# Kernel tuning notes

Hardware: AMD Instinct MI355X
Metric: run time of the kernel (lower is better)

Reference implementation:

```python
import jax, jax.numpy as jnp
import numpy as np
from jax import lax

DN = ('NCHW', 'OIHW', 'NCHW')


def conv3x3(x, w, b):
    return lax.conv_general_dilated(x, w, (1, 1), 'SAME', dimension_numbers=DN) + b[None, :, None, None]


def conv1x1(x, w, b):
    # w: [O, I] -> pointwise conv
    return jnp.einsum('oi,bihw->bohw', w, x) + b[None, :, None, None]


def sft(x0, x1, sc0w, sc0b, sc1w, sc1b, sh0w, sh0b, sh1w, sh1b):
    scale = conv1x1(jax.nn.leaky_relu(conv1x1(x1, sc0w, sc0b), 0.1), sc1w, sc1b)
    shift = conv1x1(jax.nn.leaky_relu(conv1x1(x1, sh0w, sh0b), 0.1), sh1w, sh1b)
    return x0 * (scale + 1.0) + shift


def deform_conv(x, offset, w, b):
    # torchvision DeformConv2d, 3x3, stride 1, pad 1, dilation 1, no mask.
    B, C, H, W = x.shape
    O = w.shape[0]
    K = 9
    off = offset.reshape(B, K, 2, H, W)  # (dy, dx) per kernel tap
    ki = jnp.arange(3, dtype=x.dtype) - 1.0
    ky = jnp.repeat(ki, 3)  # [9]
    kx = jnp.tile(ki, 3)
    hh = jnp.arange(H, dtype=x.dtype)
    ww = jnp.arange(W, dtype=x.dtype)
    py = off[:, :, 0] + hh[None, None, :, None] + ky[None, :, None, None]  # [B,K,H,W]
    px = off[:, :, 1] + ww[None, None, None, :] + kx[None, :, None, None]
    y0f = jnp.floor(py)
    x0f = jnp.floor(px)
    wy = (py - y0f)[:, None]  # [B,1,K,H,W]
    wx = (px - x0f)[:, None]
    y0 = y0f.astype(jnp.int32)
    x0i = x0f.astype(jnp.int32)
    x_flat = x.reshape(B, C, H * W)

    def gather(iy, ix):
        valid = (iy >= 0) & (iy < H) & (ix >= 0) & (ix < W)
        idx = (jnp.clip(iy, 0, H - 1) * W + jnp.clip(ix, 0, W - 1)).reshape(B, K * H * W)
        vals = jax.vmap(lambda xf, ii: xf[:, ii])(x_flat, idx)  # [B,C,K*H*W]
        return vals.reshape(B, C, K, H, W) * valid[:, None].astype(x.dtype)

    v00 = gather(y0, x0i)
    v01 = gather(y0, x0i + 1)
    v10 = gather(y0 + 1, x0i)
    v11 = gather(y0 + 1, x0i + 1)
    samp = (v00 * (1 - wy) * (1 - wx) + v01 * (1 - wy) * wx
            + v10 * wy * (1 - wx) + v11 * wy * wx)  # [B,C,K,H,W]
    return jnp.einsum('bckhw,ock->bohw', samp, w.reshape(O, C, K)) + b[None, :, None, None]


def setup_inputs() -> dict:
    key = jax.random.key(0)
    ks = jax.random.split(key, 32)
    B, C0, C1, H, W = 4, 128, 32, 96, 96
    f32 = jnp.float32
    d = {
        'x0': jax.random.normal(ks[0], (B, C0, H, W), f32),
        'x1': jax.random.normal(ks[1], (B, C1, H, W), f32),
        'w_off': jax.random.normal(ks[2], (18, C0, 3, 3), f32) * 0.02,
        'b_off': jnp.zeros((18,), f32),
        's1_sc0_w': jax.random.normal(ks[3], (C0, C1), f32) * 0.05,
        's1_sc0_b': jnp.zeros((C0,), f32),
        's1_sc1_w': jax.random.normal(ks[4], (C0, C0), f32) * 0.05,
        's1_sc1_b': jnp.zeros((C0,), f32),
        's1_sh0_w': jax.random.normal(ks[5], (C0, C1), f32) * 0.05,
        's1_sh0_b': jnp.zeros((C0,), f32),
        's1_sh1_w': jax.random.normal(ks[6], (C0, C0), f32) * 0.05,
        's1_sh1_b': jnp.zeros((C0,), f32),
        'w_d1': jax.random.normal(ks[7], (C0, C0, 3, 3), f32) * 0.03,
        'b_d1': jnp.zeros((C0,), f32),
        's2_sc0_w': jax.random.normal(ks[8], (C0, C1), f32) * 0.05,
        's2_sc0_b': jnp.zeros((C0,), f32),
        's2_sc1_w': jax.random.normal(ks[9], (C0, C0), f32) * 0.05,
        's2_sc1_b': jnp.zeros((C0,), f32),
        's2_sh0_w': jax.random.normal(ks[10], (C0, C1), f32) * 0.05,
        's2_sh0_b': jnp.zeros((C0,), f32),
        's2_sh1_w': jax.random.normal(ks[11], (C0, C0), f32) * 0.05,
        's2_sh1_b': jnp.zeros((C0,), f32),
        'w_d2': jax.random.normal(ks[12], (C0, C0, 3, 3), f32) * 0.03,
        'b_d2': jnp.zeros((C0,), f32),
    }
    return d


def reference(x0, x1, w_off, b_off,
              s1_sc0_w, s1_sc0_b, s1_sc1_w, s1_sc1_b,
              s1_sh0_w, s1_sh0_b, s1_sh1_w, s1_sh1_b,
              w_d1, b_d1,
              s2_sc0_w, s2_sc0_b, s2_sc1_w, s2_sc1_b,
              s2_sh0_w, s2_sh0_b, s2_sh1_w, s2_sh1_b,
              w_d2, b_d2):
    off = conv3x3(x0, w_off, b_off)
    fea = sft(x0, x1, s1_sc0_w, s1_sc0_b, s1_sc1_w, s1_sc1_b,
              s1_sh0_w, s1_sh0_b, s1_sh1_w, s1_sh1_b)
    fea = jax.nn.relu(deform_conv(fea, off, w_d1, b_d1))
    fea = sft(fea, x1, s2_sc0_w, s2_sc0_b, s2_sc1_w, s2_sc1_b,
              s2_sh0_w, s2_sh0_b, s2_sh1_w, s2_sh1_b)
    fea = deform_conv(fea, off, w_d2, b_d2)
    return x0 + fea
```

## Files before the change

kernel.cpp:

```cpp
#include <hip/hip_runtime.h>

typedef unsigned short u16;
typedef unsigned int   u32;
typedef __attribute__((ext_vector_type(8))) _Float16 f16x8;
typedef __attribute__((ext_vector_type(2))) float f32x2;
typedef __attribute__((ext_vector_type(4))) float f32x4;
typedef __attribute__((ext_vector_type(4))) unsigned int u32x4;

constexpr int B_  = 4;
constexpr int C0  = 128;
constexpr int C1  = 32;
constexpr int H_  = 96;
constexpr int W_  = 96;
constexpr int HW  = H_ * W_;
constexpr int PT  = 64;
constexpr int TPB = HW / PT;
constexpr int NTILE = B_ * TPB;

__device__ inline u16 f2h(float f) {
    _Float16 h = (_Float16)f;
    return __builtin_bit_cast(u16, h);
}

__global__ __launch_bounds__(256) void k_prep(
    const float* __restrict__ w_off,
    const float* __restrict__ wd1,  const float* __restrict__ wd2,
    const float* __restrict__ s1c0, const float* __restrict__ s1h0,
    const float* __restrict__ s2c0, const float* __restrict__ s2h0,
    const float* __restrict__ s1c1, const float* __restrict__ s1h1,
    const float* __restrict__ s2c1, const float* __restrict__ s2h1,
    float* __restrict__ wofft, u16* __restrict__ wdhi, u16* __restrict__ wdlo,
    u16* __restrict__ w0h,     u16* __restrict__ w1h)
{
    int t = blockIdx.x * 256 + threadIdx.x;
    if (t < C0 * 18 * 9) {
        int c = t / 162, r = t % 162, o = r / 9, tap = r % 9;
        wofft[t] = w_off[(o * C0 + c) * 9 + tap];
    }
    if (t < 2 * 9 * C0 * C0) {
        int d = t / (9 * C0 * C0), r = t % (9 * C0 * C0);
        int k = r / (C0 * C0), r2 = r % (C0 * C0), o = r2 / C0, c = r2 % C0;
        const float* wsrc = d ? wd2 : wd1;
        float wv = wsrc[(o * C0 + c) * 9 + k];
        _Float16 hi = (_Float16)wv;
        float rr = wv - (float)hi;
        wdhi[t] = __builtin_bit_cast(u16, hi);
        wdlo[t] = f2h(rr);
    }
    if (t < 4 * C0 * C1) {
        int m = t / (C0 * C1), i = t % (C0 * C1);
        const float* s = (m == 0) ? s1c0 : (m == 1) ? s1h0 : (m == 2) ? s2c0 : s2h0;
        w0h[t] = f2h(s[i]);
    }
    if (t < 4 * C0 * C0) {
        int m = t / (C0 * C0), i = t % (C0 * C0);
        const float* s = (m == 0) ? s1c1 : (m == 1) ? s1h1 : (m == 2) ? s2c1 : s2h1;
        w1h[t] = f2h(s[i]);
    }
}

__global__ __launch_bounds__(256) void k_conv_off(
    const float* __restrict__ x0, const float* __restrict__ wofft,
    const float* __restrict__ boff, float* __restrict__ off)
{
    int bx = blockIdx.x;
    int b  = bx / TPB;
    int p0 = (bx % TPB) * PT;
    int tid = threadIdx.x;
    int p   = tid & 63;
    int cq  = __builtin_amdgcn_readfirstlane(tid >> 6);
    int pos = p0 + p;
    int h = pos / W_, w = pos % W_;

    float acc[18];
#pragma unroll
    for (int o = 0; o < 18; ++o) acc[o] = 0.f;

    for (int cc = 0; cc < 32; ++cc) {
        int c = cq * 32 + cc;
        const float* xb = x0 + ((size_t)(b * C0 + c)) * HW;
        float v[9];
#pragma unroll
        for (int t = 0; t < 9; ++t) {
            int dy = t / 3 - 1, dx = t % 3 - 1;
            int hy = h + dy, wx = w + dx;
            bool ok = (hy >= 0) & (hy < H_) & (wx >= 0) & (wx < W_);
            v[t] = ok ? xb[hy * W_ + wx] : 0.f;
        }
        const float* wr = wofft + c * 162;
#pragma unroll
        for (int o = 0; o < 18; ++o)
#pragma unroll
            for (int t = 0; t < 9; ++t)
                acc[o] = fmaf(wr[o * 9 + t], v[t], acc[o]);
    }

    __shared__ float red[4][18][PT];
#pragma unroll
    for (int o = 0; o < 18; ++o) red[cq][o][p] = acc[o];
    __syncthreads();
    for (int idx = tid; idx < 18 * PT; idx += 256) {
        int o = idx / PT, pp = idx % PT;
        float s = red[0][o][pp] + red[1][o][pp] + red[2][o][pp] + red[3][o][pp]
                + boff[o];
        off[((size_t)(b * 18 + o)) * HW + p0 + pp] = s;
    }
}

template <int XSRC>
__global__ __launch_bounds__(512) void k_sft_mma(
    const float* __restrict__ xf,
    const float* __restrict__ xT,
    const float* __restrict__ x1,
    const u16* __restrict__ w0s, const u16* __restrict__ w0h,
    const u16* __restrict__ w1s, const u16* __restrict__ w1h,
    const float* __restrict__ b0s, const float* __restrict__ b0h,
    const float* __restrict__ b1s, const float* __restrict__ b1h,
    float* __restrict__ outT)
{
    __shared__ __align__(16) u16   x1t[64 * 32];
    __shared__ __align__(16) u16   hidt[2][64 * 128];
    __shared__ __align__(16) float outt[64 * 128];

    int bx = blockIdx.x, b = bx / TPB, p0 = (bx % TPB) * PT;
    int tid = threadIdx.x, l = tid & 63;
    int w = __builtin_amdgcn_readfirstlane(tid >> 6);
    f32x4 zz = {0.f, 0.f, 0.f, 0.f};

    for (int i = tid; i < C1 * PT; i += 512) {
        int ch = i >> 6, pos = i & 63;
        float v = x1[((size_t)(b * C1 + ch)) * HW + p0 + pos];
        x1t[pos * 32 + (ch ^ ((pos & 3) << 3))] = f2h(v);
    }
    __syncthreads();

    {
        int mt = w & 3, br = w >> 2;
        int pos = mt * 16 + (l & 15);
        int koff = (l >> 4) * 8;
        f16x8 a = *(const f16x8*)&x1t[pos * 32 + (koff ^ ((pos & 3) << 3))];
        const u16* w0 = br ? w0h : w0s;
        const float* bb = br ? b0h : b0s;
        u16* hrow = hidt[br];
#pragma unroll
        for (int nt = 0; nt < 8; ++nt) {
            int n = nt * 16 + (l & 15);
            f16x8 bfr = *(const f16x8*)&w0[n * 32 + koff];
            f32x4 h = __builtin_amdgcn_mfma_f32_16x16x32_f16(a, bfr, zz, 0, 0, 0);
            float bv = bb[n];
#pragma unroll
            for (int r = 0; r < 4; ++r) {
                float hv = h[r] + bv;
                hv = hv > 0.f ? hv : 0.1f * hv;
                int prow = mt * 16 + (l >> 4) * 4 + r;
                hrow[prow * 128 + (n ^ ((prow & 7) << 3))] = f2h(hv);
            }
        }
    }
    __syncthreads();

    f32x4 accS[4], accH[4];
#pragma unroll
    for (int nt = 0; nt < 4; ++nt) { accS[nt] = zz; accH[nt] = zz; }
    int mt = w & 3, nh = w >> 2;
    int pos = mt * 16 + (l & 15);
#pragma unroll
    for (int ks = 0; ks < 4; ++ks) {
        int kb = ks * 32 + (l >> 4) * 8;
        f16x8 aS = *(const f16x8*)&hidt[0][pos * 128 + (kb ^ ((pos & 7) << 3))];
        f16x8 aH = *(const f16x8*)&hidt[1][pos * 128 + (kb ^ ((pos & 7) << 3))];
#pragma unroll
        for (int nt = 0; nt < 4; ++nt) {
            int n = nh * 64 + nt * 16 + (l & 15);
            f16x8 bS = *(const f16x8*)&w1s[n * 128 + kb];
            f16x8 bH = *(const f16x8*)&w1h[n * 128 + kb];
            accS[nt] = __builtin_amdgcn_mfma_f32_16x16x32_f16(aS, bS, accS[nt], 0, 0, 0);
            accH[nt] = __builtin_amdgcn_mfma_f32_16x16x32_f16(aH, bH, accH[nt], 0, 0, 0);
        }
    }

#pragma unroll
    for (int nt = 0; nt < 4; ++nt) {
        int n = nh * 64 + nt * 16 + (l & 15);
        float scb = b1s[n], shb = b1h[n];
        float xv[4];
        if (XSRC == 0) {
            const float* xp = xf + ((size_t)(b * C0 + n)) * HW + p0 + mt * 16 + (l >> 4) * 4;
            f32x4 x4 = *(const f32x4*)xp;
#pragma unroll
            for (int r = 0; r < 4; ++r) xv[r] = x4[r];
        } else {
#pragma unroll
            for (int r = 0; r < 4; ++r)
                xv[r] = xT[((size_t)(b * HW + p0 + mt * 16 + (l >> 4) * 4 + r)) * C0 + n];
        }
#pragma unroll
        for (int r = 0; r < 4; ++r) {
            float scale = accS[nt][r] + scb + 1.f;
            float shift = accH[nt][r] + shb;
            outt[(mt * 16 + (l >> 4) * 4 + r) * 128 + n] = xv[r] * scale + shift;
        }
    }
    __syncthreads();

    float* dst = outT + ((size_t)(b * HW + p0)) * C0;
    for (int i = tid; i < 2048; i += 512)
        *(f32x4*)&dst[i * 4] = *(const f32x4*)&outt[i * 4];
}

template <int MODE>
__global__ __launch_bounds__(512, 4) void k_deform4(
    const float* __restrict__ srcT,
    const float* __restrict__ off,
    const u16* __restrict__ whi,
    const u16* __restrict__ wlo,
    const float* __restrict__ bias,
    const float* __restrict__ x0,
    float* __restrict__ outF,
    float* __restrict__ outT)
{
    constexpr int S = 136;
    __shared__ __align__(16) u16   smem[4 * 64 * S];
    __shared__ __align__(16) u16   cidx[9 * 64 * 4];
    __shared__ __align__(16) float cwt[9 * 64 * 2];
    u16* a_hi = smem;
    u16* a_lo = smem + 64 * S;
    u16* b_hi = smem + 2 * 64 * S;
    u16* b_lo = smem + 3 * 64 * S;

    int bx = blockIdx.x;
    bx = (bx & 7) * (NTILE / 8) + (bx >> 3);
    int b = bx / TPB, p0 = (bx % TPB) * PT;
    int tid = threadIdx.x, l = tid & 63;
    int w = __builtin_amdgcn_readfirstlane(tid >> 6);
    f32x4 zz = {0.f, 0.f, 0.f, 0.f};

    for (int e = tid; e < 9 * 64; e += 512) {
        int k = e >> 6, pp = e & 63;
        int pos = p0 + pp, h = pos / W_, wc = pos % W_;
        float dy = off[((size_t)(b * 18 + 2 * k)) * HW + pos];
        float dx = off[((size_t)(b * 18 + 2 * k + 1)) * HW + pos];
        float py = dy + (float)(h + k / 3 - 1);
        float px = dx + (float)(wc + k % 3 - 1);
        float yf = floorf(py), xf = floorf(px);
        int y0 = (int)yf, x0i = (int)xf;
        cwt[e * 2]     = py - yf;
        cwt[e * 2 + 1] = px - xf;
        int iy0 = min(max(y0, 0), H_ - 1),     iy1 = min(max(y0 + 1, 0), H_ - 1);
        int ix0 = min(max(x0i, 0), W_ - 1),    ix1 = min(max(x0i + 1, 0), W_ - 1);
        bool vy0 = (y0 >= 0) & (y0 < H_),      vy1 = (y0 + 1 >= 0) & (y0 + 1 < H_);
        bool vx0 = (x0i >= 0) & (x0i < W_),    vx1 = (x0i + 1 >= 0) & (x0i + 1 < W_);
        cidx[e * 4 + 0] = (u16)(iy0 * W_ + ix0) | ((vy0 & vx0) ? 0x8000 : 0);
        cidx[e * 4 + 1] = (u16)(iy0 * W_ + ix1) | ((vy0 & vx1) ? 0x8000 : 0);
        cidx[e * 4 + 2] = (u16)(iy1 * W_ + ix0) | ((vy1 & vx0) ? 0x8000 : 0);
        cidx[e * 4 + 3] = (u16)(iy1 * W_ + ix1) | ((vy1 & vx1) ? 0x8000 : 0);
    }
    __syncthreads();

    f32x4 acc[2][2];
#pragma unroll
    for (int hf = 0; hf < 2; ++hf)
#pragma unroll
        for (int nt = 0; nt < 2; ++nt) acc[hf][nt] = zz;

    int mt = w & 3, ng = w >> 2;
    int pos_r = mt * 16 + (l & 15);
    int so = tid >> 3, sp = tid & 7;
    const float* base  = srcT + (size_t)b * HW * C0;
    const float* lbase = base + 2 * l;

    f32x2 gv[8][4];

#define ISSUE(KK)                                                             \
    {                                                                         \
        int ek = (KK) * 64 + w * 8;                                           \
        _Pragma("unroll")                                                     \
        for (int i = 0; i < 8; ++i) {                                         \
            int e = ek + i;                                                   \
            u32 c01 = *(const u32*)&cidx[e * 4];                              \
            u32 c23 = *(const u32*)&cidx[e * 4 + 2];                          \
            gv[i][0] = *(const f32x2*)(lbase + (size_t)(c01 & 0x3fffu) * C0); \
            gv[i][1] = *(const f32x2*)(lbase + (size_t)((c01 >> 16) & 0x3fffu) * C0); \
            gv[i][2] = *(const f32x2*)(lbase + (size_t)(c23 & 0x3fffu) * C0); \
            gv[i][3] = *(const f32x2*)(lbase + (size_t)((c23 >> 16) & 0x3fffu) * C0); \
        }                                                                     \
    }

#define COMMIT(KK)                                                            \
    {                                                                         \
        int ek = (KK) * 64 + w * 8;                                           \
        _Pragma("unroll")                                                     \
        for (int i = 0; i < 8; ++i) {                                         \
            int e = ek + i, pp = w * 8 + i;                                   \
            u32 c01 = *(const u32*)&cidx[e * 4];                              \
            u32 c23 = *(const u32*)&cidx[e * 4 + 2];                          \
            float wy = cwt[e * 2], wx = cwt[e * 2 + 1];                       \
            float aa  = wy * wx;                                              \
            float w11 = (c23 & 0x80000000u) ? aa : 0.f;                       \
            float w10 = (c23 & 0x8000u) ? (wy - aa) : 0.f;                    \
            float w01 = (c01 & 0x80000000u) ? (wx - aa) : 0.f;                \
            float w00 = (c01 & 0x8000u) ? (1.f - wy - wx + aa) : 0.f;         \
            float s0 = gv[i][0][0] * w00 + gv[i][1][0] * w01                  \
                     + gv[i][2][0] * w10 + gv[i][3][0] * w11;                 \
            float s1 = gv[i][0][1] * w00 + gv[i][1][1] * w01                  \
                     + gv[i][2][1] * w10 + gv[i][3][1] * w11;                 \
            _Float16 h0 = (_Float16)s0, h1 = (_Float16)s1;                    \
            float r0 = s0 - (float)h0, r1 = s1 - (float)h1;                   \
            u32 hv = (u32)__builtin_bit_cast(u16, h0)                         \
                   | ((u32)__builtin_bit_cast(u16, h1) << 16);                \
            u32 lv = (u32)f2h(r0) | ((u32)f2h(r1) << 16);                     \
            *(u32*)&a_hi[pp * S + 2 * l] = hv;                                \
            *(u32*)&a_lo[pp * S + 2 * l] = lv;                                \
        }                                                                     \
    }

#define STAGEB(KK, HF)                                                        \
    {                                                                         \
        int orow = (HF) * 64 + so;                                            \
        const u16* sh = whi + ((size_t)(KK) * C0 + orow) * C0 + sp * 16;      \
        const u16* sl = wlo + ((size_t)(KK) * C0 + orow) * C0 + sp * 16;      \
        _Pragma("unroll")                                                     \
        for (int j = 0; j < 2; ++j) {                                         \
            *(u32x4*)&b_hi[so * S + sp * 16 + j * 8] = *(const u32x4*)&sh[j * 8]; \
            *(u32x4*)&b_lo[so * S + sp * 16 + j * 8] = *(const u32x4*)&sl[j * 8]; \
        }                                                                     \
    }

#define MFMA_HALF(HF)                                                         \
    {                                                                         \
        _Pragma("unroll")                                                     \
        for (int ks = 0; ks < 4; ++ks) {                                      \
            int kb = ks * 32 + (l >> 4) * 8;                                  \
            int ai = pos_r * S + kb;                                          \
            f16x8 ah = *(const f16x8*)&a_hi[ai];                              \
            f16x8 al = *(const f16x8*)&a_lo[ai];                              \
            _Pragma("unroll")                                                 \
            for (int nt = 0; nt < 2; ++nt) {                                  \
                int orow = ng * 32 + nt * 16 + (l & 15);                      \
                int bi = orow * S + kb;                                       \
                f16x8 bh = *(const f16x8*)&b_hi[bi];                          \
                f16x8 bl = *(const f16x8*)&b_lo[bi];                          \
                acc[HF][nt] = __builtin_amdgcn_mfma_f32_16x16x32_f16(ah, bh, acc[HF][nt], 0, 0, 0); \
                acc[HF][nt] = __builtin_amdgcn_mfma_f32_16x16x32_f16(al, bh, acc[HF][nt], 0, 0, 0); \
                acc[HF][nt] = __builtin_amdgcn_mfma_f32_16x16x32_f16(ah, bl, acc[HF][nt], 0, 0, 0); \
            }                                                                 \
        }                                                                     \
    }

    ISSUE(0)
    for (int k = 0; k < 9; ++k) {
        COMMIT(k)
        STAGEB(k, 0)
        __syncthreads();
        if (k < 8) ISSUE(k + 1)
        MFMA_HALF(0)
        __syncthreads();
        STAGEB(k, 1)
        __syncthreads();
        MFMA_HALF(1)
        __syncthreads();
    }
#undef ISSUE
#undef COMMIT
#undef STAGEB
#undef MFMA_HALF

    if (MODE == 0) {
        float* otile = (float*)smem;
#pragma unroll
        for (int hf = 0; hf < 2; ++hf)
#pragma unroll
            for (int nt = 0; nt < 2; ++nt) {
                int o = hf * 64 + ng * 32 + nt * 16 + (l & 15);
                float bv = bias[o];
#pragma unroll
                for (int r = 0; r < 4; ++r) {
                    float v = acc[hf][nt][r] + bv;
                    v = v > 0.f ? v : 0.f;
                    otile[(mt * 16 + (l >> 4) * 4 + r) * 132 + o] = v;
                }
            }
        __syncthreads();
        float* dst = outT + ((size_t)(b * HW + p0)) * C0;
        for (int i = tid; i < 2048; i += 512) {
            int row = i >> 5, c = i & 31;
            *(f32x4*)&dst[row * 128 + c * 4] = *(const f32x4*)&otile[row * 132 + c * 4];
        }
    } else {
#pragma unroll
        for (int hf = 0; hf < 2; ++hf)
#pragma unroll
            for (int nt = 0; nt < 2; ++nt) {
                int o = hf * 64 + ng * 32 + nt * 16 + (l & 15);
                float bv = bias[o];
                size_t base_o = ((size_t)(b * C0 + o)) * HW + p0 + mt * 16 + (l >> 4) * 4;
                f32x4 x4 = *(const f32x4*)(x0 + base_o);
                f32x4 ov;
#pragma unroll
                for (int r = 0; r < 4; ++r) ov[r] = acc[hf][nt][r] + bv + x4[r];
                *(f32x4*)(outF + base_o) = ov;
            }
    }
}

constexpr size_t WB_OFF   = 0;
constexpr size_t WB_WOFFT = 2654208;
constexpr size_t WB_W0H   = 2737152;
constexpr size_t WB_W1H   = 2769920;
constexpr size_t WB_WDHI  = 2900992;
constexpr size_t WB_WDLO  = 4080640;
constexpr size_t WB_TA    = 5260288;
constexpr size_t WB_TB    = 24134656;

extern "C" void kernel_launch(void* const* d_in, const int* in_sizes, int n_in,
                              void* d_out, int out_size, void* d_ws, size_t ws_size,
                              hipStream_t stream)
{
    const float* x0      = (const float*)d_in[0];
    const float* x1      = (const float*)d_in[1];
    const float* w_off   = (const float*)d_in[2];
    const float* b_off   = (const float*)d_in[3];
    const float* s1_sc0w = (const float*)d_in[4];
    const float* s1_sc0b = (const float*)d_in[5];
    const float* s1_sc1w = (const float*)d_in[6];
    const float* s1_sc1b = (const float*)d_in[7];
    const float* s1_sh0w = (const float*)d_in[8];
    const float* s1_sh0b = (const float*)d_in[9];
    const float* s1_sh1w = (const float*)d_in[10];
    const float* s1_sh1b = (const float*)d_in[11];
    const float* w_d1    = (const float*)d_in[12];
    const float* b_d1    = (const float*)d_in[13];
    const float* s2_sc0w = (const float*)d_in[14];
    const float* s2_sc0b = (const float*)d_in[15];
    const float* s2_sc1w = (const float*)d_in[16];
    const float* s2_sc1b = (const float*)d_in[17];
    const float* s2_sh0w = (const float*)d_in[18];
    const float* s2_sh0b = (const float*)d_in[19];
    const float* s2_sh1w = (const float*)d_in[20];
    const float* s2_sh1b = (const float*)d_in[21];
    const float* w_d2    = (const float*)d_in[22];
    const float* b_d2    = (const float*)d_in[23];

    char* wsb = (char*)d_ws;
    float* off   = (float*)(wsb + WB_OFF);
    float* wofft = (float*)(wsb + WB_WOFFT);
    u16*   w0h   = (u16*)(wsb + WB_W0H);
    u16*   w1h   = (u16*)(wsb + WB_W1H);
    u16*   wdhi  = (u16*)(wsb + WB_WDHI);
    u16*   wdlo  = (u16*)(wsb + WB_WDLO);
    float* TA    = (float*)(wsb + WB_TA);
    float* TB    = (float*)(wsb + WB_TB);

    k_prep<<<1152, 256, 0, stream>>>(w_off, w_d1, w_d2,
                                     s1_sc0w, s1_sh0w, s2_sc0w, s2_sh0w,
                                     s1_sc1w, s1_sh1w, s2_sc1w, s2_sh1w,
                                     wofft, wdhi, wdlo, w0h, w1h);
    k_conv_off<<<NTILE, 256, 0, stream>>>(x0, wofft, b_off, off);
    k_sft_mma<0><<<NTILE, 512, 0, stream>>>(x0, nullptr, x1,
                                            w0h, w0h + 4096,
                                            w1h, w1h + 16384,
                                            s1_sc0b, s1_sh0b, s1_sc1b, s1_sh1b, TA);
    k_deform4<0><<<NTILE, 512, 0, stream>>>(TA, off, wdhi, wdlo, b_d1,
                                            nullptr, nullptr, TB);
    k_sft_mma<1><<<NTILE, 512, 0, stream>>>(nullptr, TB, x1,
                                            w0h + 8192, w0h + 12288,
                                            w1h + 32768, w1h + 49152,
                                            s2_sc0b, s2_sh0b, s2_sc1b, s2_sh1b, TA);
    k_deform4<1><<<NTILE, 512, 0, stream>>>(TA, off, wdhi + 9 * 16384, wdlo + 9 * 16384,
                                            b_d2, x0, (float*)d_out, nullptr);
}
```

Before: 373.3 us.

## Software-pipeline deform-conv gathers and weight loads across MFMA halves

Splits the per-tap bilinear gather into two half-batches held in separate register sets and prefetches the fp16 weight tiles into registers one stage ahead. The second half of the gather and the next weight half are issued before the MFMA phases, so global-memory latency overlaps with matrix work. Scheduling barriers keep the compiler from reordering the loads past the synchronisations. This cuts the peak gather register footprint from 8 taps to two sets of 4 but adds 16 registers for weights, which may affect occupancy under the 512x4 launch bound.

```diff
diff --git a/kernel.cpp b/kernel.cpp
--- a/kernel.cpp
+++ b/kernel.cpp
@@ -209,7 +209,7 @@
 }
 
 template <int MODE>
-__global__ __launch_bounds__(512, 4) void k_deform4(
+__global__ __launch_bounds__(512, 4) void k_deform5(
     const float* __restrict__ srcT,
     const float* __restrict__ off,
     const u16* __restrict__ whi,
@@ -269,29 +269,30 @@
     const float* base  = srcT + (size_t)b * HW * C0;
     const float* lbase = base + 2 * l;
 
-    f32x2 gv[8][4];
-
-#define ISSUE(KK)                                                             \
+    f32x2 gv1[4][4], gv2[4][4];
+    u32x4 rbh0, rbh1, rbl0, rbl1;
+
+#define ISSUE_A(DST, KK, IOFF)                                                \
     {                                                                         \
-        int ek = (KK) * 64 + w * 8;                                           \
+        int ek = (KK) * 64 + w * 8 + (IOFF);                                  \
         _Pragma("unroll")                                                     \
-        for (int i = 0; i < 8; ++i) {                                         \
+        for (int i = 0; i < 4; ++i) {                                         \
             int e = ek + i;                                                   \
             u32 c01 = *(const u32*)&cidx[e * 4];                              \
             u32 c23 = *(const u32*)&cidx[e * 4 + 2];                          \
-            gv[i][0] = *(const f32x2*)(lbase + (size_t)(c01 & 0x3fffu) * C0); \
-            gv[i][1] = *(const f32x2*)(lbase + (size_t)((c01 >> 16) & 0x3fffu) * C0); \
-            gv[i][2] = *(const f32x2*)(lbase + (size_t)(c23 & 0x3fffu) * C0); \
-            gv[i][3] = *(const f32x2*)(lbase + (size_t)((c23 >> 16) & 0x3fffu) * C0); \
+            DST[i][0] = *(const f32x2*)(lbase + (size_t)(c01 & 0x3fffu) * C0);\
+            DST[i][1] = *(const f32x2*)(lbase + (size_t)((c01 >> 16) & 0x3fffu) * C0); \
+            DST[i][2] = *(const f32x2*)(lbase + (size_t)(c23 & 0x3fffu) * C0);\
+            DST[i][3] = *(const f32x2*)(lbase + (size_t)((c23 >> 16) & 0x3fffu) * C0); \
         }                                                                     \
     }
 
-#define COMMIT(KK)                                                            \
+#define COMMIT_HALF(SRC, KK, IOFF)                                            \
     {                                                                         \
-        int ek = (KK) * 64 + w * 8;                                           \
+        int ek = (KK) * 64 + w * 8 + (IOFF);                                  \
         _Pragma("unroll")                                                     \
-        for (int i = 0; i < 8; ++i) {                                         \
-            int e = ek + i, pp = w * 8 + i;                                   \
+        for (int i = 0; i < 4; ++i) {                                         \
+            int e = ek + i, pp = w * 8 + (IOFF) + i;                          \
             u32 c01 = *(const u32*)&cidx[e * 4];                              \
             u32 c23 = *(const u32*)&cidx[e * 4 + 2];                          \
             float wy = cwt[e * 2], wx = cwt[e * 2 + 1];                       \
@@ -300,10 +301,10 @@
             float w10 = (c23 & 0x8000u) ? (wy - aa) : 0.f;                    \
             float w01 = (c01 & 0x80000000u) ? (wx - aa) : 0.f;                \
             float w00 = (c01 & 0x8000u) ? (1.f - wy - wx + aa) : 0.f;         \
-            float s0 = gv[i][0][0] * w00 + gv[i][1][0] * w01                  \
-                     + gv[i][2][0] * w10 + gv[i][3][0] * w11;                 \
-            float s1 = gv[i][0][1] * w00 + gv[i][1][1] * w01                  \
-                     + gv[i][2][1] * w10 + gv[i][3][1] * w11;                 \
+            float s0 = SRC[i][0][0] * w00 + SRC[i][1][0] * w01                \
+                     + SRC[i][2][0] * w10 + SRC[i][3][0] * w11;               \
+            float s1 = SRC[i][0][1] * w00 + SRC[i][1][1] * w01                \
+                     + SRC[i][2][1] * w10 + SRC[i][3][1] * w11;               \
             _Float16 h0 = (_Float16)s0, h1 = (_Float16)s1;                    \
             float r0 = s0 - (float)h0, r1 = s1 - (float)h1;                   \
             u32 hv = (u32)__builtin_bit_cast(u16, h0)                         \
@@ -314,16 +315,21 @@
         }                                                                     \
     }
 
-#define STAGEB(KK, HF)                                                        \
+#define ISSUE_B(KK, HF)                                                       \
     {                                                                         \
         int orow = (HF) * 64 + so;                                            \
         const u16* sh = whi + ((size_t)(KK) * C0 + orow) * C0 + sp * 16;      \
         const u16* sl = wlo + ((size_t)(KK) * C0 + orow) * C0 + sp * 16;      \
-        _Pragma("unroll")                                                     \
-        for (int j = 0; j < 2; ++j) {                                         \
-            *(u32x4*)&b_hi[so * S + sp * 16 + j * 8] = *(const u32x4*)&sh[j * 8]; \
-            *(u32x4*)&b_lo[so * S + sp * 16 + j * 8] = *(const u32x4*)&sl[j * 8]; \
-        }                                                                     \
+        rbh0 = *(const u32x4*)&sh[0];  rbh1 = *(const u32x4*)&sh[8];          \
+        rbl0 = *(const u32x4*)&sl[0];  rbl1 = *(const u32x4*)&sl[8];          \
+    }
+
+#define WRITE_B()                                                             \
+    {                                                                         \
+        *(u32x4*)&b_hi[so * S + sp * 16]     = rbh0;                          \
+        *(u32x4*)&b_hi[so * S + sp * 16 + 8] = rbh1;                          \
+        *(u32x4*)&b_lo[so * S + sp * 16]     = rbl0;                          \
+        *(u32x4*)&b_lo[so * S + sp * 16 + 8] = rbl1;                          \
     }
 
 #define MFMA_HALF(HF)                                                         \
@@ -347,22 +353,32 @@
         }                                                                     \
     }
 
-    ISSUE(0)
+    ISSUE_A(gv1, 0, 0)
+    ISSUE_A(gv2, 0, 4)
+    ISSUE_B(0, 0)
+
     for (int k = 0; k < 9; ++k) {
-        COMMIT(k)
-        STAGEB(k, 0)
+        COMMIT_HALF(gv1, k, 0)
+        COMMIT_HALF(gv2, k, 4)
+        WRITE_B()
+        ISSUE_B(k, 1)
+        if (k < 8) ISSUE_A(gv1, k + 1, 0)
+        __builtin_amdgcn_sched_barrier(0);
         __syncthreads();
-        if (k < 8) ISSUE(k + 1)
         MFMA_HALF(0)
         __syncthreads();
-        STAGEB(k, 1)
+        WRITE_B()
+        if (k < 8) { ISSUE_B(k + 1, 0) }
+        if (k < 8) { ISSUE_A(gv2, k + 1, 4) }
+        __builtin_amdgcn_sched_barrier(0);
         __syncthreads();
         MFMA_HALF(1)
         __syncthreads();
     }
-#undef ISSUE
-#undef COMMIT
-#undef STAGEB
+#undef ISSUE_A
+#undef COMMIT_HALF
+#undef ISSUE_B
+#undef WRITE_B
 #undef MFMA_HALF
 
     if (MODE == 0) {
@@ -460,12 +476,12 @@
                                             w0h, w0h + 4096,
                                             w1h, w1h + 16384,
                                             s1_sc0b, s1_sh0b, s1_sc1b, s1_sh1b, TA);
-    k_deform4<0><<<NTILE, 512, 0, stream>>>(TA, off, wdhi, wdlo, b_d1,
+    k_deform5<0><<<NTILE, 512, 0, stream>>>(TA, off, wdhi, wdlo, b_d1,
                                             nullptr, nullptr, TB);
     k_sft_mma<1><<<NTILE, 512, 0, stream>>>(nullptr, TB, x1,
                                             w0h + 8192, w0h + 12288,
                                             w1h + 32768, w1h + 49152,
                                             s2_sc0b, s2_sh0b, s2_sc1b, s2_sh1b, TA);
-    k_deform4<1><<<NTILE, 512, 0, stream>>>(TA, off, wdhi + 9 * 16384, wdlo + 9 * 16384,
+    k_deform5<1><<<NTILE, 512, 0, stream>>>(TA, off, wdhi + 9 * 16384, wdlo + 9 * 16384,
                                             b_d2, x0, (float*)d_out, nullptr);
 }
```

Measured after the change: 365.2 us. -2.2%, faster.

## Double-buffer deform conv tiles with register-staged weights and fewer barriers

Applied to the files above, without the earlier changes.

The deformable conv kernel now double-buffers the gathered A tile and stages the full 128-row weight slice in LDS once per tap. Weights and gathers for tap k+2 are prefetched into registers while MFMAs run on tap k, which cuts the per-tap barrier count from four to two, and MFMA sections are raised in priority with setprio. The warp layout changes to 2x4 with 32x32 output per warp, increasing A/B fragment reuse. The SFT kernel drops its LDS output staging in favour of direct strided global stores and gets a 6-waves occupancy hint. The risks are higher LDS and register use lowering occupancy, and uncoalesced stores in the SFT kernel.

```diff
diff --git a/kernel.cpp b/kernel.cpp
--- a/kernel.cpp
+++ b/kernel.cpp
@@ -108,7 +108,7 @@
 }
 
 template <int XSRC>
-__global__ __launch_bounds__(512) void k_sft_mma(
+__global__ __launch_bounds__(512, 6) void k_sft_mma(
     const float* __restrict__ xf,
     const float* __restrict__ xT,
     const float* __restrict__ x1,
@@ -118,9 +118,8 @@
     const float* __restrict__ b1s, const float* __restrict__ b1h,
     float* __restrict__ outT)
 {
-    __shared__ __align__(16) u16   x1t[64 * 32];
-    __shared__ __align__(16) u16   hidt[2][64 * 128];
-    __shared__ __align__(16) float outt[64 * 128];
+    __shared__ __align__(16) u16 x1t[64 * 32];
+    __shared__ __align__(16) u16 hidt[2][64 * 128];
 
     int bx = blockIdx.x, b = bx / TPB, p0 = (bx % TPB) * PT;
     int tid = threadIdx.x, l = tid & 63;
@@ -198,18 +197,14 @@
         for (int r = 0; r < 4; ++r) {
             float scale = accS[nt][r] + scb + 1.f;
             float shift = accH[nt][r] + shb;
-            outt[(mt * 16 + (l >> 4) * 4 + r) * 128 + n] = xv[r] * scale + shift;
-        }
-    }
-    __syncthreads();
-
-    float* dst = outT + ((size_t)(b * HW + p0)) * C0;
-    for (int i = tid; i < 2048; i += 512)
-        *(f32x4*)&dst[i * 4] = *(const f32x4*)&outt[i * 4];
+            outT[((size_t)(b * HW + p0 + mt * 16 + (l >> 4) * 4 + r)) * C0 + n]
+                = xv[r] * scale + shift;
+        }
+    }
 }
 
 template <int MODE>
-__global__ __launch_bounds__(512, 4) void k_deform4(
+__global__ __launch_bounds__(512) void k_deform9(
     const float* __restrict__ srcT,
     const float* __restrict__ off,
     const u16* __restrict__ whi,
@@ -220,13 +215,10 @@
     float* __restrict__ outT)
 {
     constexpr int S = 136;
-    __shared__ __align__(16) u16   smem[4 * 64 * S];
+    __shared__ __align__(16) u16   a_buf[2][2][64 * S];
+    __shared__ __align__(16) u16   b_buf[2][128 * S];
     __shared__ __align__(16) u16   cidx[9 * 64 * 4];
     __shared__ __align__(16) float cwt[9 * 64 * 2];
-    u16* a_hi = smem;
-    u16* a_lo = smem + 64 * S;
-    u16* b_hi = smem + 2 * 64 * S;
-    u16* b_lo = smem + 3 * 64 * S;
 
     int bx = blockIdx.x;
     bx = (bx & 7) * (NTILE / 8) + (bx >> 3);
@@ -259,19 +251,19 @@
 
     f32x4 acc[2][2];
 #pragma unroll
-    for (int hf = 0; hf < 2; ++hf)
-#pragma unroll
-        for (int nt = 0; nt < 2; ++nt) acc[hf][nt] = zz;
-
-    int mt = w & 3, ng = w >> 2;
-    int pos_r = mt * 16 + (l & 15);
-    int so = tid >> 3, sp = tid & 7;
-    const float* base  = srcT + (size_t)b * HW * C0;
-    const float* lbase = base + 2 * l;
+    for (int ms = 0; ms < 2; ++ms)
+#pragma unroll
+        for (int ns = 0; ns < 2; ++ns) acc[ms][ns] = zz;
+
+    int mh = w & 1, ng = w >> 1;
+    int kq = l >> 4;
+    const float* lbase = srcT + (size_t)b * HW * C0 + 2 * l;
+    int wrow = tid >> 2, wseg = tid & 3;
 
     f32x2 gv[8][4];
-
-#define ISSUE(KK)                                                             \
+    u32x4 wbh[4], wbl[4];
+
+#define ISSUE_G(KK)                                                           \
     {                                                                         \
         int ek = (KK) * 64 + w * 8;                                           \
         _Pragma("unroll")                                                     \
@@ -284,9 +276,22 @@
             gv[i][2] = *(const f32x2*)(lbase + (size_t)(c23 & 0x3fffu) * C0); \
             gv[i][3] = *(const f32x2*)(lbase + (size_t)((c23 >> 16) & 0x3fffu) * C0); \
         }                                                                     \
-    }
-
-#define COMMIT(KK)                                                            \
+        __builtin_amdgcn_sched_barrier(0);                                    \
+    }
+
+#define ISSUE_W(KK)                                                           \
+    {                                                                         \
+        const u16* sh = whi + (size_t)(KK) * 16384 + wrow * 128 + wseg * 32;  \
+        const u16* sl = wlo + (size_t)(KK) * 16384 + wrow * 128 + wseg * 32;  \
+        _Pragma("unroll")                                                     \
+        for (int j = 0; j < 4; ++j) {                                         \
+            wbh[j] = *(const u32x4*)&sh[j * 8];                               \
+            wbl[j] = *(const u32x4*)&sl[j * 8];                               \
+        }                                                                     \
+        __builtin_amdgcn_sched_barrier(0);                                    \
+    }
+
+#define COMMIT_A(KK, D)                                                       \
     {                                                                         \
         int ek = (KK) * 64 + w * 8;                                           \
         _Pragma("unroll")                                                     \
@@ -309,75 +314,96 @@
             u32 hv = (u32)__builtin_bit_cast(u16, h0)                         \
                    | ((u32)__builtin_bit_cast(u16, h1) << 16);                \
             u32 lv = (u32)f2h(r0) | ((u32)f2h(r1) << 16);                     \
-            *(u32*)&a_hi[pp * S + 2 * l] = hv;                                \
-            *(u32*)&a_lo[pp * S + 2 * l] = lv;                                \
+            *(u32*)&a_buf[D][0][pp * S + 2 * l] = hv;                         \
+            *(u32*)&a_buf[D][1][pp * S + 2 * l] = lv;                         \
         }                                                                     \
     }
 
-#define STAGEB(KK, HF)                                                        \
-    {                                                                         \
-        int orow = (HF) * 64 + so;                                            \
-        const u16* sh = whi + ((size_t)(KK) * C0 + orow) * C0 + sp * 16;      \
-        const u16* sl = wlo + ((size_t)(KK) * C0 + orow) * C0 + sp * 16;      \
-        _Pragma("unroll")                                                     \
-        for (int j = 0; j < 2; ++j) {                                         \
-            *(u32x4*)&b_hi[so * S + sp * 16 + j * 8] = *(const u32x4*)&sh[j * 8]; \
-            *(u32x4*)&b_lo[so * S + sp * 16 + j * 8] = *(const u32x4*)&sl[j * 8]; \
-        }                                                                     \
-    }
-
-#define MFMA_HALF(HF)                                                         \
+#define WRITE_B()                                                             \
     {                                                                         \
         _Pragma("unroll")                                                     \
-        for (int ks = 0; ks < 4; ++ks) {                                      \
-            int kb = ks * 32 + (l >> 4) * 8;                                  \
-            int ai = pos_r * S + kb;                                          \
-            f16x8 ah = *(const f16x8*)&a_hi[ai];                              \
-            f16x8 al = *(const f16x8*)&a_lo[ai];                              \
-            _Pragma("unroll")                                                 \
-            for (int nt = 0; nt < 2; ++nt) {                                  \
-                int orow = ng * 32 + nt * 16 + (l & 15);                      \
-                int bi = orow * S + kb;                                       \
-                f16x8 bh = *(const f16x8*)&b_hi[bi];                          \
-                f16x8 bl = *(const f16x8*)&b_lo[bi];                          \
-                acc[HF][nt] = __builtin_amdgcn_mfma_f32_16x16x32_f16(ah, bh, acc[HF][nt], 0, 0, 0); \
-                acc[HF][nt] = __builtin_amdgcn_mfma_f32_16x16x32_f16(al, bh, acc[HF][nt], 0, 0, 0); \
-                acc[HF][nt] = __builtin_amdgcn_mfma_f32_16x16x32_f16(ah, bl, acc[HF][nt], 0, 0, 0); \
-            }                                                                 \
+        for (int j = 0; j < 4; ++j) {                                         \
+            *(u32x4*)&b_buf[0][wrow * S + wseg * 32 + j * 8] = wbh[j];        \
+            *(u32x4*)&b_buf[1][wrow * S + wseg * 32 + j * 8] = wbl[j];        \
         }                                                                     \
     }
 
-    ISSUE(0)
+#define MFMA_KS(KS, D)                                                        \
+    {                                                                         \
+        int kb = (KS) * 32 + kq * 8;                                          \
+        f16x8 ah0 = *(const f16x8*)&a_buf[D][0][(mh * 32 + (l & 15)) * S + kb];      \
+        f16x8 al0 = *(const f16x8*)&a_buf[D][1][(mh * 32 + (l & 15)) * S + kb];      \
+        f16x8 ah1 = *(const f16x8*)&a_buf[D][0][(mh * 32 + 16 + (l & 15)) * S + kb]; \
+        f16x8 al1 = *(const f16x8*)&a_buf[D][1][(mh * 32 + 16 + (l & 15)) * S + kb]; \
+        f16x8 bh0 = *(const f16x8*)&b_buf[0][(ng * 32 + (l & 15)) * S + kb];         \
+        f16x8 bl0 = *(const f16x8*)&b_buf[1][(ng * 32 + (l & 15)) * S + kb];         \
+        f16x8 bh1 = *(const f16x8*)&b_buf[0][(ng * 32 + 16 + (l & 15)) * S + kb];    \
+        f16x8 bl1 = *(const f16x8*)&b_buf[1][(ng * 32 + 16 + (l & 15)) * S + kb];    \
+        acc[0][0] = __builtin_amdgcn_mfma_f32_16x16x32_f16(ah0, bh0, acc[0][0], 0, 0, 0); \
+        acc[0][1] = __builtin_amdgcn_mfma_f32_16x16x32_f16(ah0, bh1, acc[0][1], 0, 0, 0); \
+        acc[1][0] = __builtin_amdgcn_mfma_f32_16x16x32_f16(ah1, bh0, acc[1][0], 0, 0, 0); \
+        acc[1][1] = __builtin_amdgcn_mfma_f32_16x16x32_f16(ah1, bh1, acc[1][1], 0, 0, 0); \
+        acc[0][0] = __builtin_amdgcn_mfma_f32_16x16x32_f16(al0, bh0, acc[0][0], 0, 0, 0); \
+        acc[0][1] = __builtin_amdgcn_mfma_f32_16x16x32_f16(al0, bh1, acc[0][1], 0, 0, 0); \
+        acc[1][0] = __builtin_amdgcn_mfma_f32_16x16x32_f16(al1, bh0, acc[1][0], 0, 0, 0); \
+        acc[1][1] = __builtin_amdgcn_mfma_f32_16x16x32_f16(al1, bh1, acc[1][1], 0, 0, 0); \
+        acc[0][0] = __builtin_amdgcn_mfma_f32_16x16x32_f16(ah0, bl0, acc[0][0], 0, 0, 0); \
+        acc[0][1] = __builtin_amdgcn_mfma_f32_16x16x32_f16(ah0, bl1, acc[0][1], 0, 0, 0); \
+        acc[1][0] = __builtin_amdgcn_mfma_f32_16x16x32_f16(ah1, bl0, acc[1][0], 0, 0, 0); \
+        acc[1][1] = __builtin_amdgcn_mfma_f32_16x16x32_f16(ah1, bl1, acc[1][1], 0, 0, 0); \
+    }
+
+#define LGKM_BAR                                                              \
+    asm volatile("s_waitcnt lgkmcnt(0)" ::: "memory");                        \
+    __builtin_amdgcn_s_barrier();
+
+    ISSUE_G(0)
+    ISSUE_W(0)
+    COMMIT_A(0, 0)
+    WRITE_B()
+    ISSUE_G(1)
+    ISSUE_W(1)
+    LGKM_BAR
+
     for (int k = 0; k < 9; ++k) {
-        COMMIT(k)
-        STAGEB(k, 0)
-        __syncthreads();
-        if (k < 8) ISSUE(k + 1)
-        MFMA_HALF(0)
-        __syncthreads();
-        STAGEB(k, 1)
-        __syncthreads();
-        MFMA_HALF(1)
-        __syncthreads();
-    }
-#undef ISSUE
-#undef COMMIT
-#undef STAGEB
-#undef MFMA_HALF
+        int d = k & 1;
+        __builtin_amdgcn_s_setprio(1);
+        MFMA_KS(0, d)
+        MFMA_KS(1, d)
+        __builtin_amdgcn_s_setprio(0);
+        if (k < 8) COMMIT_A(k + 1, d ^ 1)
+        __builtin_amdgcn_s_setprio(1);
+        MFMA_KS(2, d)
+        MFMA_KS(3, d)
+        __builtin_amdgcn_s_setprio(0);
+        LGKM_BAR
+        if (k < 8) WRITE_B()
+        if (k < 7) {
+            ISSUE_G(k + 2)
+            ISSUE_W(k + 2)
+        }
+        LGKM_BAR
+    }
+#undef ISSUE_G
+#undef ISSUE_W
+#undef COMMIT_A
+#undef WRITE_B
+#undef MFMA_KS
+#undef LGKM_BAR
 
     if (MODE == 0) {
-        float* otile = (float*)smem;
-#pragma unroll
-        for (int hf = 0; hf < 2; ++hf)
-#pragma unroll
-            for (int nt = 0; nt < 2; ++nt) {
-                int o = hf * 64 + ng * 32 + nt * 16 + (l & 15);
+        float* otile = (float*)&a_buf[0][0][0];
+#pragma unroll
+        for (int ms = 0; ms < 2; ++ms)
+#pragma unroll
+            for (int ns = 0; ns < 2; ++ns) {
+                int o = ng * 32 + ns * 16 + (l & 15);
                 float bv = bias[o];
 #pragma unroll
                 for (int r = 0; r < 4; ++r) {
-                    float v = acc[hf][nt][r] + bv;
+                    float v = acc[ms][ns][r] + bv;
                     v = v > 0.f ? v : 0.f;
-                    otile[(mt * 16 + (l >> 4) * 4 + r) * 132 + o] = v;
+                    otile[(mh * 32 + ms * 16 + (l >> 4) * 4 + r) * 132 + o] = v;
                 }
             }
         __syncthreads();
@@ -388,16 +414,17 @@
         }
     } else {
 #pragma unroll
-        for (int hf = 0; hf < 2; ++hf)
-#pragma unroll
-            for (int nt = 0; nt < 2; ++nt) {
-                int o = hf * 64 + ng * 32 + nt * 16 + (l & 15);
+        for (int ms = 0; ms < 2; ++ms)
+#pragma unroll
+            for (int ns = 0; ns < 2; ++ns) {
+                int o = ng * 32 + ns * 16 + (l & 15);
                 float bv = bias[o];
-                size_t base_o = ((size_t)(b * C0 + o)) * HW + p0 + mt * 16 + (l >> 4) * 4;
+                size_t base_o = ((size_t)(b * C0 + o)) * HW + p0
+                              + mh * 32 + ms * 16 + (l >> 4) * 4;
                 f32x4 x4 = *(const f32x4*)(x0 + base_o);
                 f32x4 ov;
 #pragma unroll
-                for (int r = 0; r < 4; ++r) ov[r] = acc[hf][nt][r] + bv + x4[r];
+                for (int r = 0; r < 4; ++r) ov[r] = acc[ms][ns][r] + bv + x4[r];
                 *(f32x4*)(outF + base_o) = ov;
             }
     }
@@ -460,12 +487,12 @@
                                             w0h, w0h + 4096,
                                             w1h, w1h + 16384,
                                             s1_sc0b, s1_sh0b, s1_sc1b, s1_sh1b, TA);
-    k_deform4<0><<<NTILE, 512, 0, stream>>>(TA, off, wdhi, wdlo, b_d1,
+    k_deform9<0><<<NTILE, 512, 0, stream>>>(TA, off, wdhi, wdlo, b_d1,
                                             nullptr, nullptr, TB);
     k_sft_mma<1><<<NTILE, 512, 0, stream>>>(nullptr, TB, x1,
                                             w0h + 8192, w0h + 12288,
                                             w1h + 32768, w1h + 49152,
                                             s2_sc0b, s2_sh0b, s2_sc1b, s2_sh1b, TA);
-    k_deform4<1><<<NTILE, 512, 0, stream>>>(TA, off, wdhi + 9 * 16384, wdlo + 9 * 16384,
+    k_deform9<1><<<NTILE, 512, 0, stream>>>(TA, off, wdhi + 9 * 16384, wdlo + 9 * 16384,
                                             b_d2, x0, (float*)d_out, nullptr);
 }
```

After: 418.4 us. 1.12x slower.
